# Performance work log

Measured on AMD Instinct MI355X. Metric: run time of the kernel, lower is better.

## Reference

```python
import jax, jax.numpy as jnp
import numpy as np
from jax import lax

BS = 64    # block size
NH = 8     # attention heads
L = 12     # layers
NEG = -1e9
EPS = 1e-12  # BigBird layer_norm_eps


def gelu_new(x):
    c = 0.7978845608028654  # sqrt(2/pi)
    return 0.5 * x * (1.0 + jnp.tanh(c * (x + 0.044715 * x * x * x)))


def layer_norm(x, s, b):
    m = jnp.mean(x, axis=-1, keepdims=True)
    v = jnp.var(x, axis=-1, keepdims=True)
    return (x - m) * lax.rsqrt(v + EPS) * s + b


def block_sparse_attn(q, k, v, mask, key_blocks):
    # q,k,v: [B,H,S,hd]; mask: [B,S] (1=keep); key_blocks: [nb-2, K] block ids
    B, H, S, hd = q.shape
    nb = S // BS
    nm = nb - 2
    K = key_blocks.shape[1]
    scale = 1.0 / np.sqrt(hd)
    qb = q.reshape(B, H, nb, BS, hd)
    kb = k.reshape(B, H, nb, BS, hd)
    vb = v.reshape(B, H, nb, BS, hd)
    mb = mask.reshape(B, nb, BS)
    # middle query blocks: attend to gathered global+window+random key blocks
    q_mid = qb[:, :, 1:-1]                                   # [B,H,nm,BS,hd]
    kg = kb[:, :, key_blocks]                                # [B,H,nm,K,BS,hd]
    vg = vb[:, :, key_blocks].reshape(B, H, nm, K * BS, hd)
    mg = mb[:, key_blocks].reshape(B, 1, nm, 1, K * BS)
    s_mid = jnp.einsum('bhnqd,bhnkzd->bhnqkz', q_mid, kg).reshape(B, H, nm, BS, K * BS)
    s_mid = s_mid * scale + NEG * (1.0 - mg)
    ctx_mid = jnp.einsum('bhnqk,bhnkd->bhnqd', jax.nn.softmax(s_mid, axis=-1), vg)
    # first/last query blocks are global: full attention rows
    q_edge = jnp.stack([qb[:, :, 0], qb[:, :, -1]], axis=2)  # [B,H,2,BS,hd]
    s_edge = jnp.einsum('bhnqd,bhkd->bhnqk', q_edge, k) * scale
    s_edge = s_edge + NEG * (1.0 - mask)[:, None, None, None, :]
    ctx_edge = jnp.einsum('bhnqk,bhkd->bhnqd', jax.nn.softmax(s_edge, axis=-1), v)
    ctx = jnp.concatenate([ctx_edge[:, :, :1], ctx_mid, ctx_edge[:, :, 1:]], axis=2)
    return ctx.reshape(B, H, S, hd)


def encoder_layer(x, p, mask, key_blocks):
    Wq, bq, Wk, bk, Wv, bv, Wo, bo, l1s, l1b, Wi_, bi_, Wo2_, bo2_, l2s, l2b = p
    B, S, Hm = x.shape
    hd = Hm // NH
    def heads(t):
        return t.reshape(B, S, NH, hd).transpose(0, 2, 1, 3)
    q = heads(x @ Wq + bq)
    k = heads(x @ Wk + bk)
    v = heads(x @ Wv + bv)
    ctx = block_sparse_attn(q, k, v, mask, key_blocks)
    ctx = ctx.transpose(0, 2, 1, 3).reshape(B, S, Hm)
    x = layer_norm(x + ctx @ Wo + bo, l1s, l1b)
    ff = gelu_new(x @ Wi_ + bi_) @ Wo2_ + bo2_
    return layer_norm(x + ff, l2s, l2b)


def forward(x, proj_w, proj_b, pos_emb, tok_emb, emb_ln_s, emb_ln_b, Wq, bq, Wk, bk, Wv, bv, Wo, bo, ln1_s, ln1_b, Wi, bi, Wo2, bo2, ln2_s, ln2_b, cw1, cb1, cw2, cb2, mask, key_blocks):
    h = x @ proj_w + proj_b                 # input projection to hidden 1536
    h = h + pos_emb[None] + tok_emb         # BigBird embeddings (token_type id 0)
    h = layer_norm(h, emb_ln_s, emb_ln_b)
    stack = (Wq, bq, Wk, bk, Wv, bv, Wo, bo, ln1_s, ln1_b, Wi, bi, Wo2, bo2, ln2_s, ln2_b)
    def body(carry, p):
        return encoder_layer(carry, p, mask, key_blocks), None
    h, _ = lax.scan(jax.checkpoint(body), h, stack)
    # replaced classifier head applied per token: Linear->ReLU->Linear
    return jnp.maximum(h @ cw1 + cb1, 0.0) @ cw2 + cb2


def setup_inputs():
    key = jax.random.key(0)
    ks = iter(jax.random.split(key, 64))
    def w(*shape):
        return jax.random.normal(next(ks), shape, jnp.float32) * 0.02
    B, S, DIN, H, FF, T = 1, 4096, 1280, 1536, 3072, 256
    nb = S // BS
    # deterministic random-block plan: per middle block, 3 random blocks
    # outside {global 0, global nb-1, window i-1..i+1}
    rng = np.random.RandomState(0)
    rows = []
    for i in range(1, nb - 1):
        fixed = [0, nb - 1, i - 1, i, i + 1]
        cand = np.setdiff1d(np.arange(nb), np.array(fixed))
        rows.append(fixed + list(rng.choice(cand, 3, replace=False)))
    key_blocks = jnp.asarray(np.array(rows, dtype=np.int32))
    z = jnp.zeros
    o = jnp.ones
    return dict(
        x=jax.random.normal(next(ks), (B, S, DIN), jnp.float32),
        proj_w=w(DIN, H), proj_b=z((H,)),
        pos_emb=w(S, H), tok_emb=w(H),
        emb_ln_s=o((H,)), emb_ln_b=z((H,)),
        Wq=w(L, H, H), bq=z((L, H)), Wk=w(L, H, H), bk=z((L, H)),
        Wv=w(L, H, H), bv=z((L, H)), Wo=w(L, H, H), bo=z((L, H)),
        ln1_s=o((L, H)), ln1_b=z((L, H)),
        Wi=w(L, H, FF), bi=z((L, FF)), Wo2=w(L, FF, H), bo2=z((L, H)),
        ln2_s=o((L, H)), ln2_b=z((L, H)),
        cw1=w(H, 512), cb1=z((512,)), cw2=w(512, T), cb2=z((T,)),
        attention_mask=jnp.ones((B, S), jnp.int32),
        key_blocks=key_blocks)


def reference(x, proj_w, proj_b, pos_emb, tok_emb, emb_ln_s, emb_ln_b, Wq, bq, Wk, bk, Wv, bv, Wo, bo, ln1_s, ln1_b, Wi, bi, Wo2, bo2, ln2_s, ln2_b, cw1, cb1, cw2, cb2, attention_mask, key_blocks):
    mask = attention_mask.astype(jnp.float32)
    return forward(x, proj_w, proj_b, pos_emb, tok_emb, emb_ln_s, emb_ln_b, Wq, bq, Wk, bk, Wv, bv, Wo, bo, ln1_s, ln1_b, Wi, bi, Wo2, bo2, ln2_s, ln2_b, cw1, cb1, cw2, cb2, mask, key_blocks)
```

## Files before the change

kernel.cpp:

```cpp
#include <hip/hip_runtime.h>

typedef unsigned short u16;
typedef unsigned int u32;
typedef __bf16 bf16x8 __attribute__((ext_vector_type(8)));
typedef float f32x4 __attribute__((ext_vector_type(4)));

#define SEQ 4096
#define HM 1536
#define QKVN 4608

__device__ inline u16 f2b(float f){
  u32 u = __builtin_bit_cast(u32, f);
  return (u16)((u + 0x7fffu + ((u>>16)&1u)) >> 16);
}
__device__ inline bf16x8 ld8(const u16* p){ return *reinterpret_cast<const bf16x8*>(p); }
__device__ inline void gload16(const void* g, void* l){
  __builtin_amdgcn_global_load_lds((const __attribute__((address_space(1))) void*)g,
                                   (__attribute__((address_space(3))) void*)l, 16, 0, 0);
}

__global__ void cvt_k(const float* __restrict__ in, u16* __restrict__ outp, int n4){
  int i = blockIdx.x*256 + threadIdx.x;
  if (i < n4){
    float4 f = reinterpret_cast<const float4*>(in)[i];
    ushort4 u; u.x=f2b(f.x); u.y=f2b(f.y); u.z=f2b(f.z); u.w=f2b(f.w);
    reinterpret_cast<ushort4*>(outp)[i] = u;
  }
}

__global__ void tconv(const float* __restrict__ W, u16* __restrict__ Wt, int K, int N){
  __shared__ float tile[32][33];
  int n0 = blockIdx.x*32, k0 = blockIdx.y*32;
  int tx = threadIdx.x, ty = threadIdx.y;
  #pragma unroll
  for (int i=0;i<4;i++){
    int kk = ty + i*8;
    tile[kk][tx] = W[(size_t)(k0+kk)*N + n0 + tx];
  }
  __syncthreads();
  #pragma unroll
  for (int i=0;i<4;i++){
    int nn = ty + i*8;
    Wt[(size_t)(n0+nn)*K + k0 + tx] = f2b(tile[tx][nn]);
  }
}

__global__ void vtrans_k(const u16* __restrict__ qkv, u16* __restrict__ vt){
  __shared__ u16 tile[32][33];
  int c0 = blockIdx.x*32, s0 = blockIdx.y*32;
  int tx = threadIdx.x, ty = threadIdx.y;
  #pragma unroll
  for (int i=0;i<4;i++)
    tile[ty+i*8][tx] = qkv[(size_t)(s0+ty+i*8)*QKVN + 3072 + c0 + tx];
  __syncthreads();
  #pragma unroll
  for (int i=0;i<4;i++)
    vt[(size_t)(c0+ty+i*8)*SEQ + s0 + tx] = tile[tx][ty+i*8];
}

__global__ void concat3_k(float* __restrict__ dst, const float* __restrict__ a,
                          const float* __restrict__ b, const float* __restrict__ c){
  int i = blockIdx.x*256 + threadIdx.x;
  if (i < 1536){ dst[i]=a[i]; dst[1536+i]=b[i]; dst[3072+i]=c[i]; }
}

template<int MODE>
__global__ __launch_bounds__(256) void gemm_k(
                       const u16* __restrict__ A, const u16* __restrict__ Bt,
                       const float* __restrict__ bias, const float* __restrict__ resid,
                       const float* __restrict__ pos, const float* __restrict__ tok,
                       u16* __restrict__ outB, float* __restrict__ outF,
                       int M, int N, int K){
  __shared__ __align__(16) u16 As[128*32];
  __shared__ __align__(16) u16 Bs[128*32];
  const int t = threadIdx.x;
  const int m0 = blockIdx.y*128, n0 = blockIdx.x*128;
  const int w = t>>6, l = t&63;
  const int wm = (w>>1)*64, wn = (w&1)*64;
  const int lr = l&15, lg = l>>4;
  const int srow = w*32 + (l>>2);
  const int scol = (l&3)*8;
  const u16* Ap = A  + (size_t)(m0 + srow)*K + scol;
  const u16* Bp = Bt + (size_t)(n0 + srow)*K + scol;
  f32x4 acc[4][4] = {};

  for (int k0 = 0; k0 < K; k0 += 32){
    #pragma unroll
    for (int i=0;i<2;i++){
      gload16(Ap + (size_t)i*16*K + k0, &As[(w*2+i)*512]);
      gload16(Bp + (size_t)i*16*K + k0, &Bs[(w*2+i)*512]);
    }
    __syncthreads();
    bf16x8 af[4], bfr[4];
    #pragma unroll
    for (int i=0;i<4;i++){
      af[i]  = ld8(&As[(wm + i*16 + lr)*32 + lg*8]);
      bfr[i] = ld8(&Bs[(wn + i*16 + lr)*32 + lg*8]);
    }
    #pragma unroll
    for (int i=0;i<4;i++)
      #pragma unroll
      for (int j=0;j<4;j++)
        acc[i][j] = __builtin_amdgcn_mfma_f32_16x16x32_bf16(af[i], bfr[j], acc[i][j], 0,0,0);
    __syncthreads();
  }

  #pragma unroll
  for (int i=0;i<4;i++){
    #pragma unroll
    for (int j=0;j<4;j++){
      int col = n0 + wn + j*16 + lr;
      float bv = bias[col];
      #pragma unroll
      for (int r2=0;r2<4;r2++){
        int row = m0 + wm + i*16 + lg*4 + r2;
        float v = acc[i][j][r2] + bv;
        size_t idx = (size_t)row*N + col;
        if (MODE==0) outB[idx] = f2b(v);
        else if (MODE==1) outF[idx] = v + resid[idx];
        else if (MODE==2){
          float g = 0.5f*v*(1.f + tanhf(0.7978845608028654f*(v + 0.044715f*v*v*v)));
          outB[idx] = f2b(g);
        }
        else if (MODE==3) outB[idx] = f2b(fmaxf(v, 0.f));
        else if (MODE==4) outF[idx] = v;
        else if (MODE==5) outF[idx] = v + pos[idx] + tok[col];
      }
    }
  }
}

__global__ void ln_k(const float* __restrict__ in, const float* __restrict__ g,
                     const float* __restrict__ bta, float* __restrict__ xf,
                     u16* __restrict__ xb){
  const int row = blockIdx.x, t = threadIdx.x;
  const float* rp = in + (size_t)row*HM;
  float v[6]; float s=0.f, s2=0.f;
  #pragma unroll
  for (int i=0;i<6;i++){ v[i] = rp[t + i*256]; s += v[i]; s2 += v[i]*v[i]; }
  #pragma unroll
  for (int o=32;o;o>>=1){ s += __shfl_down(s,o,64); s2 += __shfl_down(s2,o,64); }
  __shared__ float red[8];
  if ((t&63)==0){ red[t>>6]=s; red[4+(t>>6)]=s2; }
  __syncthreads();
  s = red[0]+red[1]+red[2]+red[3]; s2 = red[4]+red[5]+red[6]+red[7];
  float mean = s*(1.f/1536.f);
  float var  = s2*(1.f/1536.f) - mean*mean;
  float inv  = rsqrtf(var + 1e-12f);
  #pragma unroll
  for (int i=0;i<6;i++){
    int c = t + i*256;
    float y = (v[i]-mean)*inv*g[c] + bta[c];
    xf[(size_t)row*HM + c] = y;
    xb[(size_t)row*HM + c] = f2b(y);
  }
}

__device__ inline int sp_off(int row, int colu16){
  return row*256 + ((((colu16)*2) ^ ((row&7)<<4)) >> 1);
}

__global__ __launch_bounds__(256, 2) void attn_k(
    const u16* __restrict__ qkv, const u16* __restrict__ vt,
    const int* __restrict__ kblocks, const int* __restrict__ amask,
    u16* __restrict__ ctx, float* __restrict__ pO,
    float* __restrict__ pm, float* __restrict__ pl){
  __shared__ __align__(16) u16 sQ[64][200];
  __shared__ __align__(16) u16 sP[64*256];
  __shared__ float swm[4][64];
  __shared__ float swl[4][64];
  __shared__ float s_m[64];
  __shared__ float s_l[64];
  __shared__ float s_al[64];

  const int t = threadIdx.x, w = t>>6, l = t&63;
  const int lr = l&15, lg = l>>4;
  const int b = blockIdx.x;
  int h, qb, split;
  bool partial;
  if (b < 496){ h = b/62; qb = 1 + b%62; split = 0; partial = false; }
  else { int e = b-496; split = e&7; int idx = e>>3; h = idx>>1; qb = (idx&1)?63:0; partial = true; }

  {
    const u16* qg = qkv + (size_t)(qb*64)*QKVN + h*192;
    #pragma unroll
    for (int i=0;i<6;i++){
      int idx = t + i*256;
      int row = idx/24, c8 = idx%24;
      *reinterpret_cast<int4*>(&sQ[row][c8*8]) =
        *reinterpret_cast<const int4*>(qg + (size_t)row*QKVN + c8*8);
    }
  }
  if (t < 64){ s_m[t] = -3.0e38f; s_l[t] = 0.f; }
  __syncthreads();

  f32x4 accO[4][3] = {};
  const float scale = 0.07216878364870323f;

  for (int c = 0; c < 2; ++c){
    const int jj = c*4 + w;
    const int kb = partial ? (split*8 + jj) : kblocks[(qb-1)*8 + jj];
    const u16* kp = qkv + (size_t)(kb*64)*QKVN + 1536 + h*192;
    f32x4 acc[4][4] = {};
    #pragma unroll
    for (int d0=0; d0<192; d0+=32){
      bf16x8 aq[4], bk_[4];
      #pragma unroll
      for (int i=0;i<4;i++)  aq[i]  = ld8(&sQ[i*16+lr][d0+lg*8]);
      #pragma unroll
      for (int jn=0;jn<4;jn++) bk_[jn] = ld8(kp + (size_t)(jn*16+lr)*QKVN + d0 + lg*8);
      #pragma unroll
      for (int i=0;i<4;i++)
        #pragma unroll
        for (int jn=0;jn<4;jn++)
          acc[i][jn] = __builtin_amdgcn_mfma_f32_16x16x32_bf16(aq[i], bk_[jn], acc[i][jn], 0,0,0);
    }
    float mcol[4];
    #pragma unroll
    for (int jn=0;jn<4;jn++)
      mcol[jn] = -1e9f*(1.f - (float)amask[kb*64 + jn*16 + lr]);
    float rmax[4][4];
    #pragma unroll
    for (int i=0;i<4;i++)
      #pragma unroll
      for (int r2=0;r2<4;r2++){
        float mx = -3.0e38f;
        #pragma unroll
        for (int jn=0;jn<4;jn++){
          float sv = acc[i][jn][r2]*scale + mcol[jn];
          acc[i][jn][r2] = sv;
          mx = fmaxf(mx, sv);
        }
        #pragma unroll
        for (int o=1;o<16;o<<=1) mx = fmaxf(mx, __shfl_xor(mx, o, 64));
        rmax[i][r2] = mx;
      }
    if (lr == 0){
      #pragma unroll
      for (int i=0;i<4;i++)
        #pragma unroll
        for (int r2=0;r2<4;r2++)
          swm[w][i*16+lg*4+r2] = rmax[i][r2];
    }
    __syncthreads();
    if (t < 64){
      float mo = s_m[t];
      float mn = fmaxf(fmaxf(fmaxf(swm[0][t], swm[1][t]), fmaxf(swm[2][t], swm[3][t])), mo);
      s_al[t] = __expf(mo - mn);
      s_m[t]  = mn;
    }
    __syncthreads();
    #pragma unroll
    for (int i=0;i<4;i++)
      #pragma unroll
      for (int r2=0;r2<4;r2++){
        const int row = i*16 + lg*4 + r2;
        const float mrow = s_m[row];
        float ssum = 0.f;
        #pragma unroll
        for (int jn=0;jn<4;jn++){
          float p = __expf(acc[i][jn][r2] - mrow);
          ssum += p;
          sP[sp_off(row, w*64 + jn*16 + lr)] = f2b(p);
        }
        #pragma unroll
        for (int o=1;o<16;o<<=1) ssum += __shfl_xor(ssum, o, 64);
        if (lr == 0) swl[w][row] = ssum;
      }
    #pragma unroll
    for (int i=0;i<4;i++)
      #pragma unroll
      for (int r2=0;r2<4;r2++){
        float a = s_al[i*16+lg*4+r2];
        #pragma unroll
        for (int jn=0;jn<3;jn++) accO[i][jn][r2] *= a;
      }
    __syncthreads();
    if (t < 64)
      s_l[t] = s_l[t]*s_al[t] + swl[0][t]+swl[1][t]+swl[2][t]+swl[3][t];
    int kb4[4];
    #pragma unroll
    for (int idx=0;idx<4;idx++)
      kb4[idx] = partial ? (split*8 + c*4 + idx) : kblocks[(qb-1)*8 + c*4 + idx];
    #pragma unroll
    for (int ks=0; ks<8; ks++){
      bf16x8 ap[4], bv_[3];
      #pragma unroll
      for (int i=0;i<4;i++) ap[i] = ld8(&sP[sp_off(i*16+lr, ks*32 + lg*8)]);
      const int sb = kb4[ks>>1]*64 + (ks&1)*32 + lg*8;
      #pragma unroll
      for (int jn=0;jn<3;jn++)
        bv_[jn] = ld8(vt + (size_t)(h*192 + w*48 + jn*16 + lr)*SEQ + sb);
      #pragma unroll
      for (int i=0;i<4;i++)
        #pragma unroll
        for (int jn=0;jn<3;jn++)
          accO[i][jn] = __builtin_amdgcn_mfma_f32_16x16x32_bf16(ap[i], bv_[jn], accO[i][jn], 0,0,0);
    }
  }
  __syncthreads();
  if (!partial){
    #pragma unroll
    for (int i=0;i<4;i++)
      #pragma unroll
      for (int r2=0;r2<4;r2++){
        const int row = i*16+lg*4+r2;
        const float inv = 1.f / s_l[row];
        #pragma unroll
        for (int jn=0;jn<3;jn++){
          const int col = h*192 + w*48 + jn*16 + lr;
          ctx[(size_t)(qb*64+row)*HM + col] = f2b(accO[i][jn][r2] * inv);
        }
      }
  } else {
    const int e = b - 496;
    #pragma unroll
    for (int i=0;i<4;i++)
      #pragma unroll
      for (int r2=0;r2<4;r2++){
        const int row = i*16+lg*4+r2;
        #pragma unroll
        for (int jn=0;jn<3;jn++){
          const int col = w*48 + jn*16 + lr;
          pO[((size_t)e*64 + row)*192 + col] = accO[i][jn][r2];
        }
      }
    if (t < 64){ pm[e*64 + t] = s_m[t]; pl[e*64 + t] = s_l[t]; }
  }
}

__global__ void attn_comb_k(const float* __restrict__ pO, const float* __restrict__ pm,
                            const float* __restrict__ pl, u16* __restrict__ ctx){
  const int b = blockIdx.x;
  const int h = b>>1, qb = (b&1)?63:0;
  const int t = threadIdx.x;
  __shared__ float sA[8][64];
  __shared__ float sInv[64];
  if (t < 64){
    float mv[8]; float M = -3.0e38f;
    #pragma unroll
    for (int s=0;s<8;s++){ mv[s] = pm[(b*8+s)*64 + t]; M = fmaxf(M, mv[s]); }
    float L = 0.f;
    #pragma unroll
    for (int s=0;s<8;s++){
      float a = __expf(mv[s]-M);
      sA[s][t] = a;
      L += pl[(b*8+s)*64 + t]*a;
    }
    sInv[t] = 1.f/L;
  }
  __syncthreads();
  #pragma unroll
  for (int i=0;i<48;i++){
    int idx = t + i*256;
    int row = idx/192, col = idx%192;
    float acc = 0.f;
    #pragma unroll
    for (int s=0;s<8;s++)
      acc += sA[s][row] * pO[((size_t)(b*8+s)*64 + row)*192 + col];
    ctx[(size_t)(qb*64+row)*HM + h*192 + col] = f2b(acc * sInv[row]);
  }
}

extern "C" void kernel_launch(void* const* d_in, const int* in_sizes, int n_in,
                              void* d_out, int out_size, void* d_ws, size_t ws_size,
                              hipStream_t stream){
  const float* x       = (const float*)d_in[0];
  const float* proj_w  = (const float*)d_in[1];
  const float* proj_b  = (const float*)d_in[2];
  const float* pos_emb = (const float*)d_in[3];
  const float* tok_emb = (const float*)d_in[4];
  const float* embs    = (const float*)d_in[5];
  const float* embb    = (const float*)d_in[6];
  const float* Wq  = (const float*)d_in[7];
  const float* bq  = (const float*)d_in[8];
  const float* Wk  = (const float*)d_in[9];
  const float* bk  = (const float*)d_in[10];
  const float* Wv  = (const float*)d_in[11];
  const float* bv  = (const float*)d_in[12];
  const float* Wo  = (const float*)d_in[13];
  const float* bo  = (const float*)d_in[14];
  const float* l1s = (const float*)d_in[15];
  const float* l1b = (const float*)d_in[16];
  const float* Wi  = (const float*)d_in[17];
  const float* bi  = (const float*)d_in[18];
  const float* Wo2 = (const float*)d_in[19];
  const float* bo2 = (const float*)d_in[20];
  const float* l2s = (const float*)d_in[21];
  const float* l2b = (const float*)d_in[22];
  const float* cw1 = (const float*)d_in[23];
  const float* cb1 = (const float*)d_in[24];
  const float* cw2 = (const float*)d_in[25];
  const float* cb2 = (const float*)d_in[26];
  const int* amask = (const int*)d_in[27];
  const int* kblk  = (const int*)d_in[28];
  float* out = (float*)d_out;

  char* base = (char*)d_ws;
  size_t off = 0;
  auto carve = [&](size_t bytes)->char*{
    char* p = base + off; off += (bytes + 255) & ~(size_t)255; return p;
  };
  float* xf32  = (float*)carve(4096ULL*1536*4);
  float* preln = (float*)carve(4096ULL*1536*4);
  u16*   xbf   = (u16*)  carve(4096ULL*1536*2);
  u16*   xinbf = (u16*)  carve(4096ULL*1280*2);
  u16*   qkv   = (u16*)  carve(4096ULL*4608*2);
  u16*   vt    = (u16*)  carve(1536ULL*4096*2);
  u16*   ctx   = (u16*)  carve(4096ULL*1536*2);
  u16*   ff1   = (u16*)  carve(4096ULL*3072*2);
  u16*   cls1  = (u16*)  carve(4096ULL*512*2);
  u16*   wt    = (u16*)  carve(4608ULL*1536*2);
  float* b3    = (float*)carve(4608ULL*4);
  float* pO    = (float*)carve(128ULL*64*192*4);
  float* pm    = (float*)carve(128ULL*64*4);
  float* pl    = (float*)carve(128ULL*64*4);
  if (off > ws_size) return;

  const dim3 tb32(32,8);

  cvt_k<<<5120, 256, 0, stream>>>(x, xinbf, 4096*1280/4);
  tconv<<<dim3(48,40), tb32, 0, stream>>>(proj_w, wt, 1280, 1536);
  gemm_k<5><<<dim3(12,32), 256, 0, stream>>>(xinbf, wt, proj_b, nullptr, pos_emb, tok_emb,
                                             nullptr, preln, 4096, 1536, 1280);
  ln_k<<<4096, 256, 0, stream>>>(preln, embs, embb, xf32, xbf);

  for (int l = 0; l < 12; ++l){
    const float* wq  = Wq  + (size_t)l*1536*1536;
    const float* wk  = Wk  + (size_t)l*1536*1536;
    const float* wv  = Wv  + (size_t)l*1536*1536;
    const float* wo  = Wo  + (size_t)l*1536*1536;
    const float* wi  = Wi  + (size_t)l*1536*3072;
    const float* wo2 = Wo2 + (size_t)l*3072*1536;
    const float* bql = bq  + (size_t)l*1536;
    const float* bkl = bk  + (size_t)l*1536;
    const float* bvl = bv  + (size_t)l*1536;
    const float* bol = bo  + (size_t)l*1536;
    const float* bil = bi  + (size_t)l*3072;
    const float* bo2l= bo2 + (size_t)l*1536;
    const float* g1  = l1s + (size_t)l*1536;
    const float* be1 = l1b + (size_t)l*1536;
    const float* g2  = l2s + (size_t)l*1536;
    const float* be2 = l2b + (size_t)l*1536;

    tconv<<<dim3(48,48), tb32, 0, stream>>>(wq, wt,                  1536, 1536);
    tconv<<<dim3(48,48), tb32, 0, stream>>>(wk, wt + 1536ULL*1536,   1536, 1536);
    tconv<<<dim3(48,48), tb32, 0, stream>>>(wv, wt + 2ULL*1536*1536, 1536, 1536);
    concat3_k<<<6, 256, 0, stream>>>(b3, bql, bkl, bvl);
    gemm_k<0><<<dim3(36,32), 256, 0, stream>>>(xbf, wt, b3, nullptr, nullptr, nullptr,
                                               qkv, nullptr, 4096, 4608, 1536);
    vtrans_k<<<dim3(48,128), tb32, 0, stream>>>(qkv, vt);

    attn_k<<<624, 256, 0, stream>>>(qkv, vt, kblk, amask, ctx, pO, pm, pl);
    attn_comb_k<<<16, 256, 0, stream>>>(pO, pm, pl, ctx);

    tconv<<<dim3(48,48), tb32, 0, stream>>>(wo, wt, 1536, 1536);
    gemm_k<1><<<dim3(12,32), 256, 0, stream>>>(ctx, wt, bol, xf32, nullptr, nullptr,
                                               nullptr, preln, 4096, 1536, 1536);
    ln_k<<<4096, 256, 0, stream>>>(preln, g1, be1, xf32, xbf);

    tconv<<<dim3(96,48), tb32, 0, stream>>>(wi, wt, 1536, 3072);
    gemm_k<2><<<dim3(24,32), 256, 0, stream>>>(xbf, wt, bil, nullptr, nullptr, nullptr,
                                               ff1, nullptr, 4096, 3072, 1536);
    tconv<<<dim3(48,96), tb32, 0, stream>>>(wo2, wt, 3072, 1536);
    gemm_k<1><<<dim3(12,32), 256, 0, stream>>>(ff1, wt, bo2l, xf32, nullptr, nullptr,
                                               nullptr, preln, 4096, 1536, 3072);
    ln_k<<<4096, 256, 0, stream>>>(preln, g2, be2, xf32, xbf);
  }

  tconv<<<dim3(16,48), tb32, 0, stream>>>(cw1, wt, 1536, 512);
  gemm_k<3><<<dim3(4,32), 256, 0, stream>>>(xbf, wt, cb1, nullptr, nullptr, nullptr,
                                            cls1, nullptr, 4096, 512, 1536);
  tconv<<<dim3(8,16), tb32, 0, stream>>>(cw2, wt, 512, 256);
  gemm_k<4><<<dim3(2,32), 256, 0, stream>>>(cls1, wt, cb2, nullptr, nullptr, nullptr,
                                            nullptr, out, 4096, 256, 512);

  (void)in_sizes; (void)n_in; (void)out_size;
}
```

Before: 5.442 ms.

## Prefetch V tiles early in attention, vectorize layernorm, merge QKV weight conversions

In the attention kernel, all V-transpose fragments for a chunk are now loaded into registers right after the QK MFMA loop, before the softmax work. This gives the global-load latency time to hide behind the softmax computation, at the cost of 24 extra bf16x8 registers, which may raise register pressure under launch_bounds(256,2). Layernorm now reads and writes float2 and packed bf16 pairs instead of scalars. The three QKV weight transpose-conversion launches are merged into one 3D-grid launch.

```diff
diff --git a/kernel.cpp b/kernel.cpp
--- a/kernel.cpp
+++ b/kernel.cpp
@@ -42,6 +42,26 @@
   for (int i=0;i<4;i++){
     int nn = ty + i*8;
     Wt[(size_t)(n0+nn)*K + k0 + tx] = f2b(tile[tx][nn]);
+  }
+}
+
+__global__ void tconv3(const float* __restrict__ W0, const float* __restrict__ W1,
+                       const float* __restrict__ W2, u16* __restrict__ Wt){
+  __shared__ float tile[32][33];
+  const float* W = (blockIdx.z==0) ? W0 : (blockIdx.z==1 ? W1 : W2);
+  u16* dst = Wt + (size_t)blockIdx.z*1536*1536;
+  int n0 = blockIdx.x*32, k0 = blockIdx.y*32;
+  int tx = threadIdx.x, ty = threadIdx.y;
+  #pragma unroll
+  for (int i=0;i<4;i++){
+    int kk = ty + i*8;
+    tile[kk][tx] = W[(size_t)(k0+kk)*1536 + n0 + tx];
+  }
+  __syncthreads();
+  #pragma unroll
+  for (int i=0;i<4;i++){
+    int nn = ty + i*8;
+    dst[(size_t)(n0+nn)*1536 + k0 + tx] = f2b(tile[tx][nn]);
   }
 }
 
@@ -134,10 +154,13 @@
                      const float* __restrict__ bta, float* __restrict__ xf,
                      u16* __restrict__ xb){
   const int row = blockIdx.x, t = threadIdx.x;
-  const float* rp = in + (size_t)row*HM;
-  float v[6]; float s=0.f, s2=0.f;
-  #pragma unroll
-  for (int i=0;i<6;i++){ v[i] = rp[t + i*256]; s += v[i]; s2 += v[i]*v[i]; }
+  const float2* rp = reinterpret_cast<const float2*>(in + (size_t)row*HM);
+  float2 v[3]; float s=0.f, s2=0.f;
+  #pragma unroll
+  for (int i=0;i<3;i++){
+    v[i] = rp[t + i*256];
+    s += v[i].x + v[i].y; s2 += v[i].x*v[i].x + v[i].y*v[i].y;
+  }
   #pragma unroll
   for (int o=32;o;o>>=1){ s += __shfl_down(s,o,64); s2 += __shfl_down(s2,o,64); }
   __shared__ float red[8];
@@ -147,12 +170,17 @@
   float mean = s*(1.f/1536.f);
   float var  = s2*(1.f/1536.f) - mean*mean;
   float inv  = rsqrtf(var + 1e-12f);
-  #pragma unroll
-  for (int i=0;i<6;i++){
-    int c = t + i*256;
-    float y = (v[i]-mean)*inv*g[c] + bta[c];
-    xf[(size_t)row*HM + c] = y;
-    xb[(size_t)row*HM + c] = f2b(y);
+  float2* xfp = reinterpret_cast<float2*>(xf + (size_t)row*HM);
+  u32*    xbp = reinterpret_cast<u32*>(xb + (size_t)row*HM);
+  #pragma unroll
+  for (int i=0;i<3;i++){
+    int c2 = t + i*256;
+    float2 gg = reinterpret_cast<const float2*>(g)[c2];
+    float2 bb = reinterpret_cast<const float2*>(bta)[c2];
+    float y0 = (v[i].x-mean)*inv*gg.x + bb.x;
+    float y1 = (v[i].y-mean)*inv*gg.y + bb.y;
+    xfp[c2] = make_float2(y0, y1);
+    xbp[c2] = (u32)f2b(y0) | ((u32)f2b(y1) << 16);
   }
 }
 
@@ -198,8 +226,11 @@
   const float scale = 0.07216878364870323f;
 
   for (int c = 0; c < 2; ++c){
-    const int jj = c*4 + w;
-    const int kb = partial ? (split*8 + jj) : kblocks[(qb-1)*8 + jj];
+    int kb4[4];
+    #pragma unroll
+    for (int idx=0;idx<4;idx++)
+      kb4[idx] = partial ? (split*8 + c*4 + idx) : kblocks[(qb-1)*8 + c*4 + idx];
+    const int kb = kb4[w];
     const u16* kp = qkv + (size_t)(kb*64)*QKVN + 1536 + h*192;
     f32x4 acc[4][4] = {};
     #pragma unroll
@@ -214,6 +245,14 @@
         #pragma unroll
         for (int jn=0;jn<4;jn++)
           acc[i][jn] = __builtin_amdgcn_mfma_f32_16x16x32_bf16(aq[i], bk_[jn], acc[i][jn], 0,0,0);
+    }
+    bf16x8 bvx[8][3];
+    #pragma unroll
+    for (int ks=0; ks<8; ks++){
+      const int sb = kb4[ks>>1]*64 + (ks&1)*32 + lg*8;
+      #pragma unroll
+      for (int jn=0;jn<3;jn++)
+        bvx[ks][jn] = ld8(vt + (size_t)(h*192 + w*48 + jn*16 + lr)*SEQ + sb);
     }
     float mcol[4];
     #pragma unroll
@@ -278,24 +317,16 @@
     __syncthreads();
     if (t < 64)
       s_l[t] = s_l[t]*s_al[t] + swl[0][t]+swl[1][t]+swl[2][t]+swl[3][t];
-    int kb4[4];
-    #pragma unroll
-    for (int idx=0;idx<4;idx++)
-      kb4[idx] = partial ? (split*8 + c*4 + idx) : kblocks[(qb-1)*8 + c*4 + idx];
     #pragma unroll
     for (int ks=0; ks<8; ks++){
-      bf16x8 ap[4], bv_[3];
+      bf16x8 ap[4];
       #pragma unroll
       for (int i=0;i<4;i++) ap[i] = ld8(&sP[sp_off(i*16+lr, ks*32 + lg*8)]);
-      const int sb = kb4[ks>>1]*64 + (ks&1)*32 + lg*8;
-      #pragma unroll
-      for (int jn=0;jn<3;jn++)
-        bv_[jn] = ld8(vt + (size_t)(h*192 + w*48 + jn*16 + lr)*SEQ + sb);
       #pragma unroll
       for (int i=0;i<4;i++)
         #pragma unroll
         for (int jn=0;jn<3;jn++)
-          accO[i][jn] = __builtin_amdgcn_mfma_f32_16x16x32_bf16(ap[i], bv_[jn], accO[i][jn], 0,0,0);
+          accO[i][jn] = __builtin_amdgcn_mfma_f32_16x16x32_bf16(ap[i], bvx[ks][jn], accO[i][jn], 0,0,0);
     }
   }
   __syncthreads();
@@ -443,9 +474,7 @@
     const float* g2  = l2s + (size_t)l*1536;
     const float* be2 = l2b + (size_t)l*1536;
 
-    tconv<<<dim3(48,48), tb32, 0, stream>>>(wq, wt,                  1536, 1536);
-    tconv<<<dim3(48,48), tb32, 0, stream>>>(wk, wt + 1536ULL*1536,   1536, 1536);
-    tconv<<<dim3(48,48), tb32, 0, stream>>>(wv, wt + 2ULL*1536*1536, 1536, 1536);
+    tconv3<<<dim3(48,48,3), tb32, 0, stream>>>(wq, wk, wv, wt);
     concat3_k<<<6, 256, 0, stream>>>(b3, bql, bkl, bvl);
     gemm_k<0><<<dim3(36,32), 256, 0, stream>>>(xbf, wt, b3, nullptr, nullptr, nullptr,
                                                qkv, nullptr, 4096, 4608, 1536);
```

Result: slower. 6.104 ms (+12.1%).
